# Kernel optimization log

Hardware: AMD Instinct MI355X
Metric: run time of the kernel (lower is better)

Reference implementation:

```python
import jax, jax.numpy as jnp
import numpy as np

B, N, H, DK, DV = 2, 2048, 16, 128, 128
E = H * DV
EPS = 1e-6


def setup_inputs() -> dict:
    key = jax.random.key(0)
    ks = jax.random.split(key, 8)
    sc_qk = 1.0 / np.sqrt(E + H * DK)  # xavier_normal-ish std
    sc_e = 1.0 / np.sqrt(2 * E)
    d = {
        "x": jax.random.normal(ks[0], (B, N, E), jnp.float32),
        "Wq": jax.random.normal(ks[1], (H * DK, E), jnp.float32) * sc_qk,
        "bq": jnp.zeros((H * DK,), jnp.float32),
        "Wk": jax.random.normal(ks[2], (H * DK, E), jnp.float32) * sc_qk,
        "bk": jnp.zeros((H * DK,), jnp.float32),
        "Wv": jax.random.normal(ks[3], (E, E), jnp.float32) * sc_e,
        "bv": jnp.zeros((E,), jnp.float32),
        "Wg": jax.random.normal(ks[4], (E, E), jnp.float32) * sc_e,
        "bg": jnp.zeros((E,), jnp.float32),
        "Wo": jax.random.normal(ks[5], (E, E), jnp.float32) * sc_e,
        "bo": jnp.zeros((E,), jnp.float32),
        "start_idx": 0,
    }
    return d


def _retention_scan(q, k, v, decays):
    # q,k: [B,N,H,DK] (k already scaled), v: [B,N,H,DV]
    qs = jnp.moveaxis(q, 1, 0)  # [N,B,H,DK]
    ks_ = jnp.moveaxis(k, 1, 0)
    vs = jnp.moveaxis(v, 1, 0)
    dec = decays[None, :, None, None]  # [1,H,1,1]

    def step(state, qkv):
        qt, kt, vt = qkv
        # state_n = decay * state_{n-1} + k_n (x) v_n
        state = dec * state + kt[..., :, None] * vt[..., None, :]  # [B,H,DK,DV]
        ret = jnp.einsum("bhk,bhkv->bhv", qt, state)
        return state, ret

    init = jnp.zeros((q.shape[0], H, DK, DV), q.dtype)
    final_state, rets = jax.lax.scan(step, init, (qs, ks_, vs))
    return jnp.moveaxis(rets, 0, 1), final_state  # [B,N,H,DV], [B,H,DK,DV]


def reference(x, Wq, bq, Wk, bk, Wv, bv, Wg, bg, Wo, bo, start_idx):
    b, n, _ = x.shape
    decays = 1.0 - jnp.exp2(-5.0 - jnp.arange(H, dtype=jnp.float32))  # [H]
    q = (x @ Wq.T + bq).reshape(b, n, H, DK)
    k = (x @ Wk.T + bk).reshape(b, n, H, DK) / (DK ** 0.5)
    v = (x @ Wv.T + bv).reshape(b, n, H, DV)
    retention, state = _retention_scan(q, k, v, decays)
    # GroupNorm over (b n) tokens, num_groups=H, channels=E, no affine
    r = retention.reshape(b * n, H, DV).astype(jnp.float32)
    mu = jnp.mean(r, axis=-1, keepdims=True)
    var = jnp.var(r, axis=-1, keepdims=True)
    r = (r - mu) / jnp.sqrt(var + EPS)
    r = r.reshape(b, n, E).astype(x.dtype)
    gate = jax.nn.silu(x @ Wg.T + bg)
    out = (r * gate) @ Wo.T + bo
    return out, state
```

## Files before the change

kernel.cpp:

```cpp
#include <hip/hip_runtime.h>
#include <hip/hip_bf16.h>

typedef __attribute__((ext_vector_type(8))) short short8;
typedef __attribute__((ext_vector_type(4))) short short4v;
typedef __attribute__((ext_vector_type(4))) float floatx4;

#define DI __device__ __forceinline__

constexpr int B_ = 2, N_ = 2048, H_ = 16, DK_ = 128, DV_ = 128, E_ = 2048;
constexpr int M_ = B_ * N_;
constexpr int NCAT_ = 4 * E_;
constexpr int CH_ = 128;
constexpr int NC_ = N_ / CH_;
constexpr float KSCALE = 0.08838834764831845f;

constexpr long OFF_XB   = 0;
constexpr long OFF_WCAT = 16777216;
constexpr long OFF_WOB  = 50331648;
constexpr long OFF_BCAT = 58720256;
constexpr long OFF_Y    = 58753024;
constexpr long OFF_VT   = 142639104;
constexpr long OFF_SCB  = 159416320;

DI unsigned short f2bf(float f){
  unsigned u = __float_as_uint(f);
  u += 0x7fffu + ((u >> 16) & 1u);
  return (unsigned short)(u >> 16);
}
DI float bf2f(unsigned short s){ return __uint_as_float(((unsigned)s) << 16); }

DI void gload_lds16(const void* g, void* l){
  __builtin_amdgcn_global_load_lds(
      (const __attribute__((address_space(1))) unsigned int*)g,
      (__attribute__((address_space(3))) unsigned int*)l, 16, 0, 0);
}

__global__ void k_castall(const float* __restrict__ x,
                          const float* __restrict__ Wq, const float* __restrict__ Wk,
                          const float* __restrict__ Wv, const float* __restrict__ Wg,
                          const float* __restrict__ Wo,
                          const float* __restrict__ bq, const float* __restrict__ bk,
                          const float* __restrict__ bv, const float* __restrict__ bg,
                          unsigned short* __restrict__ xb, unsigned short* __restrict__ Wcat,
                          unsigned short* __restrict__ Wob, float* __restrict__ bcat){
  int bid = blockIdx.x;
  if(bid >= 14336){
    int i = (bid - 14336) * 2048 + threadIdx.x * 8;
    #pragma unroll
    for(int u=0;u<8;++u){
      int j = i + u;
      float v;
      if(j < 2048)      v = bq[j];
      else if(j < 4096) v = bk[j - 2048];
      else if(j < 6144) v = bv[j - 4096];
      else              v = bg[j - 6144];
      bcat[j] = v;
    }
    return;
  }
  const float* s; unsigned short* d; long off;
  if(bid < 4096){ s = x; d = xb; off = (long)bid*2048; }
  else if(bid < 6144){ s = Wq; d = Wcat;            off = (long)(bid-4096)*2048; }
  else if(bid < 8192){ s = Wk; d = Wcat + 4194304L; off = (long)(bid-6144)*2048; }
  else if(bid < 10240){ s = Wv; d = Wcat + 8388608L; off = (long)(bid-8192)*2048; }
  else if(bid < 12288){ s = Wg; d = Wcat + 12582912L; off = (long)(bid-10240)*2048; }
  else { s = Wo; d = Wob; off = (long)(bid-12288)*2048; }
  long i = off + (long)threadIdx.x * 8;
  float4 v0 = *(const float4*)(s + i);
  float4 v1 = *(const float4*)(s + i + 4);
  short8 o;
  o[0]=(short)f2bf(v0.x); o[1]=(short)f2bf(v0.y); o[2]=(short)f2bf(v0.z); o[3]=(short)f2bf(v0.w);
  o[4]=(short)f2bf(v1.x); o[5]=(short)f2bf(v1.y); o[6]=(short)f2bf(v1.z); o[7]=(short)f2bf(v1.w);
  *(short8*)(d + i) = o;
}

__global__ __launch_bounds__(512, 2)
void k_gemm256(const unsigned short* __restrict__ A,
               const unsigned short* __restrict__ Bt,
               unsigned short* __restrict__ Y,
               const float* __restrict__ bias)
{
  extern __shared__ unsigned short lds[];
  constexpr int K = 2048;
  constexpr int NKT = K / 64;

  const int tid = threadIdx.x;
  const int wave = tid >> 6, lane = tid & 63;
  const int wr = wave >> 2, wc = wave & 3;
  const int l15 = lane & 15;

  int bid = blockIdx.x;
  int g = bid & 7, w = bid >> 3;
  int bm = (g & 1) * 8 + (w & 7);
  int bn = (g >> 1) * 8 + (w >> 3);

  const unsigned short* Ag = A  + (long)bm * 256 * K;
  const unsigned short* Bg = Bt + (long)bn * 256 * K;

  const int sr = (lane >> 3);
  const int sc = ((lane & 7) ^ sr) * 8;
  const int colx[2] = { ((0 + (lane>>4)) ^ (lane&7)) << 4,
                        ((4 + (lane>>4)) ^ (lane&7)) << 4 };

  floatx4 acc[8][4] = {};
  const char* ldsc = (const char*)lds;
  short8 Aa[8], Ab[8], Ba[4], Bb[4];

#define STG_A(buf, kt, mh) do{                                                        \
    _Pragma("unroll")                                                                 \
    for(int g2=0; g2<2; ++g2){                                                        \
      gload_lds16(Ag + (long)(wr*128 + (mh)*64 + wc*16 + g2*8 + sr)*K                 \
                     + (long)(kt)*64 + sc,                                            \
                  &lds[(buf)*16384 + wr*8192 + ((mh)*64 + wc*16 + g2*8)*64 + lane*8]);\
    }                                                                                 \
  }while(0)

#define STG_B(buf, kt, nh) do{                                                        \
    _Pragma("unroll")                                                                 \
    for(int g2=0; g2<2; ++g2){                                                        \
      gload_lds16(Bg + (long)(wc*64 + (nh)*32 + wr*16 + g2*8 + sr)*K                  \
                     + (long)(kt)*64 + sc,                                            \
                  &lds[32768 + (buf)*16384 + (wc>>1)*8192                             \
                       + ((wc&1)*64 + (nh)*32 + wr*16 + g2*8)*64 + lane*8]);          \
    }                                                                                 \
  }while(0)

#define RD_A(dst, buf, mh) do{                                                        \
    const char* _b = ldsc + ((buf)*16384 + wr*8192)*2;                                \
    _Pragma("unroll")                                                                 \
    for(int ai=0; ai<4; ++ai){                                                        \
      const int _rb = ((mh)*64 + ai*16 + l15) << 7;                                   \
      dst[ai*2+0] = *(const short8*)(_b + _rb + colx[0]);                             \
      dst[ai*2+1] = *(const short8*)(_b + _rb + colx[1]);                             \
    }                                                                                 \
  }while(0)

#define RD_B(dst, buf, nh) do{                                                        \
    const char* _b = ldsc + (32768 + (buf)*16384 + (wc>>1)*8192)*2;                   \
    _Pragma("unroll")                                                                 \
    for(int bj=0; bj<2; ++bj){                                                        \
      const int _rb = ((wc&1)*64 + (nh)*32 + bj*16 + l15) << 7;                       \
      dst[bj*2+0] = *(const short8*)(_b + _rb + colx[0]);                             \
      dst[bj*2+1] = *(const short8*)(_b + _rb + colx[1]);                             \
    }                                                                                 \
  }while(0)

#define MFQ(mh, nh, As, Bs) do{                                                       \
    __builtin_amdgcn_s_setprio(1);                                                    \
    _Pragma("unroll")                                                                 \
    for(int ai=0; ai<4; ++ai)                                                         \
      _Pragma("unroll")                                                               \
      for(int bj=0; bj<2; ++bj)                                                       \
        _Pragma("unroll")                                                             \
        for(int kk=0; kk<2; ++kk)                                                     \
          acc[(mh)*4+ai][(nh)*2+bj] = __builtin_amdgcn_mfma_f32_16x16x32_bf16(        \
              As[ai*2+kk], Bs[bj*2+kk], acc[(mh)*4+ai][(nh)*2+bj], 0,0,0);            \
    __builtin_amdgcn_s_setprio(0);                                                    \
  }while(0)

#define VM4   asm volatile("s_waitcnt vmcnt(4)" ::: "memory")
#define BAR   __builtin_amdgcn_s_barrier()
#define SCHED __builtin_amdgcn_sched_barrier(0)

  STG_A(0, 0, 0); STG_B(0, 0, 0); STG_B(0, 0, 1); STG_A(0, 0, 1);
  VM4;
  BAR;
  SCHED;

  #pragma unroll 1
  for(int i=0; i<NKT/2; ++i){
    const int t1 = 2*i + 1;
    const int t2 = (2*i + 2) & (NKT - 1);

    RD_A(Aa, 0, 0); RD_B(Ba, 0, 0);
    STG_A(1, t1, 0); STG_B(1, t1, 0);
    VM4; BAR;
    MFQ(0, 0, Aa, Ba);
    BAR; SCHED;
    RD_B(Bb, 0, 1);
    STG_B(1, t1, 1);
    VM4; BAR;
    MFQ(0, 1, Aa, Bb);
    BAR; SCHED;
    RD_A(Ab, 0, 1);
    STG_A(1, t1, 1);
    VM4; BAR;
    MFQ(1, 1, Ab, Bb);
    BAR; SCHED;
    VM4; BAR;
    MFQ(1, 0, Ab, Ba);
    BAR; SCHED;

    RD_A(Aa, 1, 0); RD_B(Ba, 1, 0);
    STG_A(0, t2, 0); STG_B(0, t2, 0);
    VM4; BAR;
    MFQ(0, 0, Aa, Ba);
    BAR; SCHED;
    RD_B(Bb, 1, 1);
    STG_B(0, t2, 1);
    VM4; BAR;
    MFQ(0, 1, Aa, Bb);
    BAR; SCHED;
    RD_A(Ab, 1, 1);
    STG_A(0, t2, 1);
    VM4; BAR;
    MFQ(1, 1, Ab, Bb);
    BAR; SCHED;
    VM4; BAR;
    MFQ(1, 0, Ab, Ba);
    BAR; SCHED;
  }
#undef STG_A
#undef STG_B
#undef RD_A
#undef RD_B
#undef MFQ
#undef VM4
#undef BAR
#undef SCHED

  #pragma unroll
  for(int mh=0;mh<2;++mh){
    #pragma unroll
    for(int ai=0;ai<4;++ai){
      const int rowi = bm*256 + wr*128 + mh*64 + ai*16 + ((lane>>4)<<2);
      #pragma unroll
      for(int nh=0;nh<2;++nh){
        #pragma unroll
        for(int bj=0;bj<2;++bj){
          const int col = bn*256 + wc*64 + nh*32 + bj*16 + l15;
          const float bs = bias[col];
          const int sec = col >> 11;
          #pragma unroll
          for(int r=0;r<4;++r){
            float v = acc[mh*4+ai][nh*2+bj][r] + bs;
            if(sec == 1) v *= KSCALE;
            else if(sec == 3) v = v / (1.f + __expf(-v));
            Y[(long)(rowi + r) * NCAT_ + col] = f2bf(v);
          }
        }
      }
    }
  }
}

__global__ __launch_bounds__(512, 2)
void k_gemm2(const unsigned short* __restrict__ A,
             const unsigned short* __restrict__ Bt,
             float* __restrict__ outp,
             const float* __restrict__ bias)
{
  extern __shared__ unsigned short lds[];
  constexpr int K = 2048;
  constexpr int NKT = K / 64;

  const int tid = threadIdx.x;
  const int wave = tid >> 6, lane = tid & 63;
  const int wm = wave >> 1, wn = wave & 1;
  const int l15 = lane & 15;

  int bid = blockIdx.x;
  int g = bid & 7, w = bid >> 3;
  int bm = (g & 1) * 8 + (w & 7);
  int bn = (g >> 1) * 4 + (w >> 3);

  const unsigned short* Ag = A  + (long)bm * 256 * K;
  const unsigned short* Bg = Bt + (long)bn * 128 * K;

  const int sr = lane >> 3;
  const int sc = ((lane & 7) ^ sr) * 8;
  const int colx[2] = { (((lane>>4)  ) ^ (lane&7)) << 4,
                        (((lane>>4)+4) ^ (lane&7)) << 4 };

  floatx4 acc[4][4] = {};
  const char* ldsc = (const char*)lds;
  short8 Av[8], Bv[4], Bw[4];

#define STG_AB(buf, kt) do{                                                           \
    _Pragma("unroll")                                                                 \
    for(int g2=0; g2<4; ++g2){                                                        \
      gload_lds16(Ag + (long)(wm*64 + wn*32 + g2*8 + sr)*K + (long)(kt)*64 + sc,      \
                  &lds[(buf)*16384 + (wm*64 + wn*32 + g2*8)*64 + lane*8]);            \
    }                                                                                 \
    _Pragma("unroll")                                                                 \
    for(int g2=0; g2<2; ++g2){                                                        \
      gload_lds16(Bg + (long)(wn*64 + wm*16 + g2*8 + sr)*K + (long)(kt)*64 + sc,      \
                  &lds[32768 + (buf)*8192 + (wn*64 + wm*16 + g2*8)*64 + lane*8]);     \
    }                                                                                 \
  }while(0)

#define RD_A2(buf) do{                                                                \
    const char* _b = ldsc + (buf)*32768;                                              \
    _Pragma("unroll")                                                                 \
    for(int ai=0; ai<4; ++ai){                                                        \
      const int _rb = (wm*64 + ai*16 + l15) << 7;                                     \
      Av[ai*2+0] = *(const short8*)(_b + _rb + colx[0]);                              \
      Av[ai*2+1] = *(const short8*)(_b + _rb + colx[1]);                              \
    }                                                                                 \
  }while(0)

#define RD_B2(dst, buf, half) do{                                                     \
    const char* _b = ldsc + 65536 + (buf)*16384;                                      \
    _Pragma("unroll")                                                                 \
    for(int bj=0; bj<2; ++bj){                                                        \
      const int _rb = (wn*64 + ((half)*2+bj)*16 + l15) << 7;                          \
      dst[bj*2+0] = *(const short8*)(_b + _rb + colx[0]);                             \
      dst[bj*2+1] = *(const short8*)(_b + _rb + colx[1]);                             \
    }                                                                                 \
  }while(0)

#define MF8(half, Bs) do{                                                             \
    __builtin_amdgcn_s_setprio(1);                                                    \
    _Pragma("unroll")                                                                 \
    for(int ai=0; ai<4; ++ai)                                                         \
      _Pragma("unroll")                                                               \
      for(int bj=0; bj<2; ++bj)                                                       \
        _Pragma("unroll")                                                             \
        for(int kk=0; kk<2; ++kk)                                                     \
          acc[ai][(half)*2+bj] = __builtin_amdgcn_mfma_f32_16x16x32_bf16(             \
              Av[ai*2+kk], Bs[bj*2+kk], acc[ai][(half)*2+bj], 0,0,0);                 \
    __builtin_amdgcn_s_setprio(0);                                                    \
  }while(0)

#define VM6   asm volatile("s_waitcnt vmcnt(6)" ::: "memory")
#define BAR   __builtin_amdgcn_s_barrier()
#define SCHED __builtin_amdgcn_sched_barrier(0)

  STG_AB(0, 0);

  #pragma unroll 1
  for(int i=0; i<NKT/2; ++i){
    const int u = 2*i;
    STG_AB(1, u+1);
    VM6; BAR;
    RD_A2(0); RD_B2(Bv, 0, 0);
    MF8(0, Bv);
    SCHED;
    RD_B2(Bw, 0, 1);
    MF8(1, Bw);
    BAR; SCHED;
    STG_AB(0, (u+2) & (NKT-1));
    VM6; BAR;
    RD_A2(1); RD_B2(Bv, 1, 0);
    MF8(0, Bv);
    SCHED;
    RD_B2(Bw, 1, 1);
    MF8(1, Bw);
    BAR; SCHED;
  }
#undef STG_AB
#undef RD_A2
#undef RD_B2
#undef MF8
#undef VM6
#undef BAR
#undef SCHED

  #pragma unroll
  for(int ai=0;ai<4;++ai){
    const int row = bm*256 + wm*64 + ai*16 + ((lane>>4)<<2);
    #pragma unroll
    for(int bj=0;bj<4;++bj){
      const int col = bn*128 + wn*64 + bj*16 + l15;
      const float bs = bias[col];
      #pragma unroll
      for(int r=0;r<4;++r)
        outp[(long)(row + r)*E_ + col] = acc[ai][bj][r] + bs;
    }
  }
}

__global__ __launch_bounds__(256)
void k_chunksumT(const unsigned short* __restrict__ Y,
                 unsigned short* __restrict__ Vt,
                 unsigned short* __restrict__ MS){
  __shared__ unsigned short lt[64][136];
  __shared__ unsigned short Kt2[128][72];
  __shared__ unsigned short Vt2[128][72];
  int bid = blockIdx.x;
  int bh = bid >> 4, c = bid & 15, b = bh >> 4, h = bh & 15;
  int tid = threadIdx.x, wave = tid >> 6, lane = tid & 63;
  int wr = wave >> 1, wc = wave & 1;
  float dec = 1.f - exp2f(-5.f - (float)h);
  float l2d = log2f(dec);

  floatx4 acc[4][4] = {};

  #pragma unroll 1
  for(int h2 = 0; h2 < 2; ++h2){
    #pragma unroll
    for(int p=0;p<4;++p){
      int tl = p*16 + (tid>>4);
      int t  = h2*64 + tl;
      long row = ((long)(b*N_ + c*CH_ + t))*NCAT_ + 2048 + h*128 + (tid&15)*8;
      short8 v = *(const short8*)(Y + row);
      float f = exp2f(-(float)t * l2d);
      #pragma unroll
      for(int u=0;u<8;++u) v[u] = (short)f2bf(bf2f((unsigned short)v[u]) * f);
      *(short8*)&lt[tl][(tid&15)*8] = v;
    }
    __syncthreads();
    #pragma unroll
    for(int p=0;p<4;++p){
      int dk = p*32 + (tid>>3);
      int tc = (tid&7)*8;
      short8 o;
      #pragma unroll
      for(int u=0;u<8;++u) o[u] = (short)lt[tc+u][dk];
      *(short8*)&Kt2[dk][tc] = o;
    }
    __syncthreads();
    #pragma unroll
    for(int p=0;p<4;++p){
      int tl = p*16 + (tid>>4);
      int t  = h2*64 + tl;
      long row = ((long)(b*N_ + c*CH_ + t))*NCAT_ + 4096 + h*128 + (tid&15)*8;
      *(short8*)&lt[tl][(tid&15)*8] = *(const short8*)(Y + row);
    }
    __syncthreads();
    #pragma unroll
    for(int p=0;p<4;++p){
      int dv = p*32 + (tid>>3);
      int tc = (tid&7)*8;
      short8 o;
      #pragma unroll
      for(int u=0;u<8;++u) o[u] = (short)lt[tc+u][dv];
      *(short8*)&Vt2[dv][tc] = o;
      *(short8*)(Vt + ((long)(bh*128 + dv))*N_ + c*CH_ + h2*64 + tc) = o;
    }
    __syncthreads();
    #pragma unroll
    for(int kk=0;kk<2;++kk){
      int tl = kk*32 + ((lane>>4)<<3);
      short8 af[4], bfr[4];
      #pragma unroll
      for(int i=0;i<4;++i){ int dv = (wr<<6)+(i<<4)+(lane&15); af[i]  = *(const short8*)&Vt2[dv][tl]; }
      #pragma unroll
      for(int j=0;j<4;++j){ int dk = (wc<<6)+(j<<4)+(lane&15); bfr[j] = *(const short8*)&Kt2[dk][tl]; }
      #pragma unroll
      for(int i=0;i<4;++i)
        #pragma unroll
        for(int j=0;j<4;++j)
          acc[i][j] = __builtin_amdgcn_mfma_f32_16x16x32_bf16(af[i], bfr[j], acc[i][j], 0,0,0);
    }
    __syncthreads();
  }

  float scale = exp2f(127.f * log2f(dec));
  unsigned short* Mo = MS + ((long)bh*NC_ + c) * 16384;
  #pragma unroll
  for(int i=0;i<4;++i)
    #pragma unroll
    for(int j=0;j<4;++j)
      #pragma unroll
      for(int r=0;r<4;++r){
        int dv = (wr<<6)+(i<<4)+((lane>>4)<<2)+r;
        int dk = (wc<<6)+(j<<4)+(lane&15);
        Mo[dv*128 + dk] = f2bf(acc[i][j][r] * scale);
      }
}

__global__ __launch_bounds__(256)
void k_scan(const unsigned short* __restrict__ MS, unsigned short* __restrict__ Scb,
            float* __restrict__ stateOut){
  int bid = blockIdx.x;
  int bh = bid >> 4, p = bid & 15;
  int tid = threadIdx.x, h = bh & 15;
  float dec = 1.f - exp2f(-5.f - (float)h);
  float decC = exp2f(128.f * log2f(dec));
  int e0 = p*1024 + tid*4;
  floatx4 S = {0.f, 0.f, 0.f, 0.f};
  const unsigned short* base = MS + (long)bh * NC_ * 16384 + e0;
  unsigned short* sb = Scb + (long)bh * NC_ * 16384 + e0;
  for(int c=0;c<NC_;++c){
    short4v m = *(const short4v*)(base + (long)c*16384);
    short4v q;
    #pragma unroll
    for(int u=0;u<4;++u) q[u] = (short)f2bf(S[u]);
    *(short4v*)(sb + (long)c*16384) = q;
    #pragma unroll
    for(int u=0;u<4;++u) S[u] = decC * S[u] + bf2f((unsigned short)m[u]);
  }
  int dv = e0 >> 7, dk = e0 & 127;
  float* so = stateOut + (long)bh*16384 + dv;
  #pragma unroll
  for(int u=0;u<4;++u) so[(long)(dk+u)*128] = S[u];
}

__global__ __launch_bounds__(256)
void k_ret(const unsigned short* __restrict__ Y, const unsigned short* __restrict__ Vt,
           const unsigned short* __restrict__ Scb, unsigned short* __restrict__ RG){
  __shared__ unsigned short sQ[128*128];
  __shared__ unsigned short sK[128*128];
  int bid = blockIdx.x;
  int bh = bid >> 4, c = bid & 15, b = bh >> 4, h = bh & 15;
  int tid = threadIdx.x, w = tid >> 6, lane = tid & 63;
  float dec = 1.f - exp2f(-5.f - (float)h);
  float l2d = log2f(dec);

  #pragma unroll
  for(int p=0;p<8;++p){
    int t = p*16 + (tid>>4);
    long row = (long)(b*N_ + c*CH_ + t) * NCAT_ + h*128 + (tid&15)*8;
    short8 qv = *(const short8*)(Y + row);
    short8 kv = *(const short8*)(Y + row + 2048);
    float fq = exp2f((float)t * l2d);
    float fk = exp2f(-(float)t * l2d);
    short8 qs, ks;
    #pragma unroll
    for(int u=0;u<8;++u){
      qs[u] = (short)f2bf(bf2f((unsigned short)qv[u]) * fq);
      ks[u] = (short)f2bf(bf2f((unsigned short)kv[u]) * fk);
    }
    int ad = t*256 + (((tid&15)*16) ^ ((t&7)<<4));
    *(short8*)((char*)sQ + ad) = qs;
    *(short8*)((char*)sK + ad) = ks;
  }
  __syncthreads();

  floatx4 acc[2][8] = {};
  #pragma unroll
  for(int kk=0;kk<4;++kk){
    int cb = (kk<<6) + ((lane>>4)<<4);
    short8 af[2], bfr[8];
    #pragma unroll
    for(int i=0;i<2;++i){ int t = w*32 + (i<<4) + (lane&15); af[i] = *(const short8*)((const char*)sQ + t*256 + (cb ^ ((t&7)<<4))); }
    #pragma unroll
    for(int j=0;j<8;++j){ int s = (j<<4) + (lane&15); bfr[j] = *(const short8*)((const char*)sK + s*256 + (cb ^ ((s&7)<<4))); }
    #pragma unroll
    for(int i=0;i<2;++i)
      #pragma unroll
      for(int j=0;j<8;++j)
        acc[i][j] = __builtin_amdgcn_mfma_f32_16x16x32_bf16(af[i], bfr[j], acc[i][j], 0,0,0);
  }
  __syncthreads();

  #pragma unroll
  for(int i=0;i<2;++i)
    #pragma unroll
    for(int j=0;j<8;++j)
      #pragma unroll
      for(int r=0;r<4;++r){
        int t = w*32 + (i<<4) + ((lane>>4)<<2) + r;
        int s = (j<<4) + (lane&15);
        float v = (s <= t) ? acc[i][j][r] : 0.f;
        *(unsigned short*)((char*)sK + t*256 + ((s*2) ^ ((t&7)<<4))) = f2bf(v);
      }
  __syncthreads();

  #pragma unroll
  for(int i=0;i<2;++i)
    #pragma unroll
    for(int j=0;j<8;++j)
      #pragma unroll
      for(int u=0;u<4;++u) acc[i][j][u] = 0.f;

  const unsigned short* Vb = Vt + (long)bh*128*N_ + c*CH_;
  #pragma unroll
  for(int kk=0;kk<4;++kk){
    int cb = (kk<<6) + ((lane>>4)<<4);
    int sg = kk*32 + ((lane>>4)<<3);
    short8 af[2], bfr[8];
    #pragma unroll
    for(int i=0;i<2;++i){ int t = w*32 + (i<<4) + (lane&15); af[i] = *(const short8*)((const char*)sK + t*256 + (cb ^ ((t&7)<<4))); }
    #pragma unroll
    for(int j=0;j<8;++j){ int dv = (j<<4) + (lane&15); bfr[j] = *(const short8*)(Vb + (long)dv*N_ + sg); }
    #pragma unroll
    for(int i=0;i<2;++i)
      #pragma unroll
      for(int j=0;j<8;++j)
        acc[i][j] = __builtin_amdgcn_mfma_f32_16x16x32_bf16(af[i], bfr[j], acc[i][j], 0,0,0);
  }
  const unsigned short* Sb = Scb + ((long)bh*NC_ + c) * 16384;
  #pragma unroll
  for(int kk=0;kk<4;++kk){
    int cb = (kk<<6) + ((lane>>4)<<4);
    int kg = kk*32 + ((lane>>4)<<3);
    short8 af[2], bfr[8];
    #pragma unroll
    for(int i=0;i<2;++i){
      int t = w*32 + (i<<4) + (lane&15);
      short8 qv = *(const short8*)((const char*)sQ + t*256 + (cb ^ ((t&7)<<4)));
      #pragma unroll
      for(int u=0;u<8;++u) af[i][u] = (short)f2bf(bf2f((unsigned short)qv[u]) * dec);
    }
    #pragma unroll
    for(int j=0;j<8;++j){ int dv = (j<<4) + (lane&15); bfr[j] = *(const short8*)(Sb + (long)dv*128 + kg); }
    #pragma unroll
    for(int i=0;i<2;++i)
      #pragma unroll
      for(int j=0;j<8;++j)
        acc[i][j] = __builtin_amdgcn_mfma_f32_16x16x32_bf16(af[i], bfr[j], acc[i][j], 0,0,0);
  }

  #pragma unroll
  for(int i=0;i<2;++i){
    #pragma unroll
    for(int r=0;r<4;++r){
      float s1 = 0.f, s2 = 0.f;
      #pragma unroll
      for(int j=0;j<8;++j){ float v = acc[i][j][r]; s1 += v; s2 += v*v; }
      #pragma unroll
      for(int off=1; off<16; off<<=1){ s1 += __shfl_xor(s1, off); s2 += __shfl_xor(s2, off); }
      float mu  = s1 * (1.f/128.f);
      float var = s2 * (1.f/128.f) - mu*mu;
      float inv = rsqrtf(var + 1e-6f);
      int t = w*32 + (i<<4) + ((lane>>4)<<2) + r;
      long mrow = (long)(b*N_ + c*CH_ + t);
      #pragma unroll
      for(int j=0;j<8;++j){
        int dv = (j<<4) + (lane&15);
        float v = (acc[i][j][r] - mu) * inv;
        float g = bf2f(Y[mrow*NCAT_ + 6144 + h*128 + dv]);
        RG[mrow*E_ + h*128 + dv] = f2bf(v * g);
      }
    }
  }
}

extern "C" void kernel_launch(void* const* d_in, const int* in_sizes, int n_in,
                              void* d_out, int out_size, void* d_ws, size_t ws_size,
                              hipStream_t stream) {
  const float* x  = (const float*)d_in[0];
  const float* Wq = (const float*)d_in[1];
  const float* bq = (const float*)d_in[2];
  const float* Wk = (const float*)d_in[3];
  const float* bk = (const float*)d_in[4];
  const float* Wv = (const float*)d_in[5];
  const float* bv = (const float*)d_in[6];
  const float* Wg = (const float*)d_in[7];
  const float* bg = (const float*)d_in[8];
  const float* Wo = (const float*)d_in[9];
  const float* bo = (const float*)d_in[10];

  char* ws = (char*)d_ws;
  unsigned short* xb   = (unsigned short*)(ws + OFF_XB);
  unsigned short* Wcat = (unsigned short*)(ws + OFF_WCAT);
  unsigned short* Wob  = (unsigned short*)(ws + OFF_WOB);
  float*          bcat = (float*)(ws + OFF_BCAT);
  unsigned short* Y    = (unsigned short*)(ws + OFF_Y);
  unsigned short* Vt   = (unsigned short*)(ws + OFF_VT);
  unsigned short* Scb  = (unsigned short*)(ws + OFF_SCB);
  unsigned short* MS   = (unsigned short*)(ws + OFF_WCAT);
  unsigned short* RG   = (unsigned short*)(ws + OFF_XB);

  float* outp     = (float*)d_out;
  float* stateOut = outp + (long)M_ * E_;

  (void)hipFuncSetAttribute((const void*)k_gemm256,
                            hipFuncAttributeMaxDynamicSharedMemorySize, 131072);
  (void)hipFuncSetAttribute((const void*)k_gemm2,
                            hipFuncAttributeMaxDynamicSharedMemorySize, 98304);

  k_castall<<<14340, 256, 0, stream>>>(x, Wq, Wk, Wv, Wg, Wo, bq, bk, bv, bg,
                                       xb, Wcat, Wob, bcat);

  k_gemm256<<<512, 512, 131072, stream>>>(xb, Wcat, Y, bcat);

  k_chunksumT<<<512, 256, 0, stream>>>(Y, Vt, MS);

  k_scan<<<512, 256, 0, stream>>>(MS, Scb, stateOut);

  k_ret<<<512, 256, 0, stream>>>(Y, Vt, Scb, RG);

  k_gemm2<<<256, 512, 98304, stream>>>(RG, Wob, outp, bo);
}
```

Baseline: 252.7 us.

## Fold intra-chunk decay scaling of Q and K into the projection GEMM epilogue

The projection GEMM epilogue now multiplies Q by decay^t and K by decay^-t, with t the position within the chunk. This removes the per-element unpack, scale and repack in k_chunksumT and k_ret, and k_ret can then load Q/K straight into LDS with direct global-to-LDS loads using a swizzled source index. k_scan is also widened to 8 elements per thread over half as many blocks. The risk is that Y now holds pre-scaled Q/K, so every consumer must agree; the k_ret Q scaling relative to any cross-chunk state term needs checking.

```diff
diff --git a/kernel.cpp b/kernel.cpp
--- a/kernel.cpp
+++ b/kernel.cpp
@@ -231,10 +231,14 @@
           const int col = bn*256 + wc*64 + nh*32 + bj*16 + l15;
           const float bs = bias[col];
           const int sec = col >> 11;
+          float l2d = 0.f;
+          if(sec <= 1) l2d = log2f(1.f - exp2f(-5.f - (float)((col >> 7) & 15)));
           #pragma unroll
           for(int r=0;r<4;++r){
             float v = acc[mh*4+ai][nh*2+bj][r] + bs;
-            if(sec == 1) v *= KSCALE;
+            const float e = (float)((rowi + r) & 127);
+            if(sec == 0)      v *= exp2f(e * l2d);
+            else if(sec == 1) v *= KSCALE * exp2f(-e * l2d);
             else if(sec == 3) v = v / (1.f + __expf(-v));
             Y[(long)(rowi + r) * NCAT_ + col] = f2bf(v);
           }
@@ -382,7 +386,6 @@
   int tid = threadIdx.x, wave = tid >> 6, lane = tid & 63;
   int wr = wave >> 1, wc = wave & 1;
   float dec = 1.f - exp2f(-5.f - (float)h);
-  float l2d = log2f(dec);
 
   floatx4 acc[4][4] = {};
 
@@ -393,11 +396,7 @@
       int tl = p*16 + (tid>>4);
       int t  = h2*64 + tl;
       long row = ((long)(b*N_ + c*CH_ + t))*NCAT_ + 2048 + h*128 + (tid&15)*8;
-      short8 v = *(const short8*)(Y + row);
-      float f = exp2f(-(float)t * l2d);
-      #pragma unroll
-      for(int u=0;u<8;++u) v[u] = (short)f2bf(bf2f((unsigned short)v[u]) * f);
-      *(short8*)&lt[tl][(tid&15)*8] = v;
+      *(short8*)&lt[tl][(tid&15)*8] = *(const short8*)(Y + row);
     }
     __syncthreads();
     #pragma unroll
@@ -464,27 +463,28 @@
 void k_scan(const unsigned short* __restrict__ MS, unsigned short* __restrict__ Scb,
             float* __restrict__ stateOut){
   int bid = blockIdx.x;
-  int bh = bid >> 4, p = bid & 15;
+  int bh = bid >> 3, p = bid & 7;
   int tid = threadIdx.x, h = bh & 15;
   float dec = 1.f - exp2f(-5.f - (float)h);
   float decC = exp2f(128.f * log2f(dec));
-  int e0 = p*1024 + tid*4;
-  floatx4 S = {0.f, 0.f, 0.f, 0.f};
+  int e0 = p*2048 + tid*8;
+  float S[8] = {};
   const unsigned short* base = MS + (long)bh * NC_ * 16384 + e0;
   unsigned short* sb = Scb + (long)bh * NC_ * 16384 + e0;
   for(int c=0;c<NC_;++c){
-    short4v m = *(const short4v*)(base + (long)c*16384);
-    short4v q;
-    #pragma unroll
-    for(int u=0;u<4;++u) q[u] = (short)f2bf(S[u]);
-    *(short4v*)(sb + (long)c*16384) = q;
-    #pragma unroll
-    for(int u=0;u<4;++u) S[u] = decC * S[u] + bf2f((unsigned short)m[u]);
+    short8 m = *(const short8*)(base + (long)c*16384);
+    short8 q;
+    #pragma unroll
+    for(int u=0;u<8;++u){
+      q[u] = (short)f2bf(S[u]);
+      S[u] = decC * S[u] + bf2f((unsigned short)m[u]);
+    }
+    *(short8*)(sb + (long)c*16384) = q;
   }
   int dv = e0 >> 7, dk = e0 & 127;
   float* so = stateOut + (long)bh*16384 + dv;
   #pragma unroll
-  for(int u=0;u<4;++u) so[(long)(dk+u)*128] = S[u];
+  for(int u=0;u<8;++u) so[(long)(dk+u)*128] = S[u];
 }
 
 __global__ __launch_bounds__(256)
@@ -496,25 +496,16 @@
   int bh = bid >> 4, c = bid & 15, b = bh >> 4, h = bh & 15;
   int tid = threadIdx.x, w = tid >> 6, lane = tid & 63;
   float dec = 1.f - exp2f(-5.f - (float)h);
-  float l2d = log2f(dec);
 
   #pragma unroll
   for(int p=0;p<8;++p){
     int t = p*16 + (tid>>4);
-    long row = (long)(b*N_ + c*CH_ + t) * NCAT_ + h*128 + (tid&15)*8;
-    short8 qv = *(const short8*)(Y + row);
-    short8 kv = *(const short8*)(Y + row + 2048);
-    float fq = exp2f((float)t * l2d);
-    float fk = exp2f(-(float)t * l2d);
-    short8 qs, ks;
-    #pragma unroll
-    for(int u=0;u<8;++u){
-      qs[u] = (short)f2bf(bf2f((unsigned short)qv[u]) * fq);
-      ks[u] = (short)f2bf(bf2f((unsigned short)kv[u]) * fk);
-    }
-    int ad = t*256 + (((tid&15)*16) ^ ((t&7)<<4));
-    *(short8*)((char*)sQ + ad) = qs;
-    *(short8*)((char*)sK + ad) = ks;
+    int cs = (lane & 15) ^ (t & 7);
+    long src = (long)(b*N_ + c*CH_ + t) * NCAT_ + h*128 + cs*8;
+    char* dq = (char*)sQ + p*4096 + (tid>>4)*256 + (lane & 15)*16;
+    char* dk = (char*)sK + p*4096 + (tid>>4)*256 + (lane & 15)*16;
+    gload_lds16(Y + src,        dq);
+    gload_lds16(Y + src + 2048, dk);
   }
   __syncthreads();
 
@@ -659,7 +650,7 @@
 
   k_chunksumT<<<512, 256, 0, stream>>>(Y, Vt, MS);
 
-  k_scan<<<512, 256, 0, stream>>>(MS, Scb, stateOut);
+  k_scan<<<256, 256, 0, stream>>>(MS, Scb, stateOut);
 
   k_ret<<<512, 256, 0, stream>>>(Y, Vt, Scb, RG);
 
```

New measurement: 258.3 us. 2.2% more time.
